# Kernel optimization log

Measured on AMD Instinct MI355X. Metric: run time of the kernel, lower is better.

## Reference

```python
import jax, jax.numpy as jnp
import numpy as np

B, T, S, L = 1, 2048, 512, 1024
C, H, Hk, D = 2048, 16, 4, 128
THETA = 10000.0


def setup_inputs() -> dict:
    key = jax.random.key(0)
    ks = jax.random.split(key, 9)
    sd = 0.02
    return {
        "x": jax.random.normal(ks[0], (B, T, C), jnp.float32),
        "stm": jax.random.normal(ks[1], (B, S, C), jnp.float32),
        "long_q": jax.random.normal(ks[2], (B, L, H, D), jnp.float32),
        "long_k": jax.random.normal(ks[3], (B, L, Hk, D), jnp.float32),
        "long_v": jax.random.normal(ks[4], (B, L, Hk, D), jnp.float32),
        "Wq": jax.random.normal(ks[5], (C, C), jnp.float32) * sd,
        "Wk": jax.random.normal(ks[6], (C, Hk * D), jnp.float32) * sd,
        "Wv": jax.random.normal(ks[7], (C, Hk * D), jnp.float32) * sd,
        "Wo": jax.random.normal(ks[8], (C, C), jnp.float32) * sd,
    }


def _rope_cos_sin(n, d, theta):
    # precompute_freqs_cis: freqs over even dims, angles t*freq
    freqs = 1.0 / (theta ** (jnp.arange(0, d, 2, dtype=jnp.float32) / d))
    ang = jnp.arange(n, dtype=jnp.float32)[:, None] * freqs[None, :]  # (n, d/2)
    return jnp.cos(ang), jnp.sin(ang)


def _apply_rope(x, cos, sin):
    # x: (B, n, h, D); complex-pair rotation over consecutive dims
    x1, x2 = x[..., 0::2], x[..., 1::2]
    c = cos[None, :, None, :]
    s = sin[None, :, None, :]
    r1 = x1 * c - x2 * s
    r2 = x1 * s + x2 * c
    return jnp.stack([r1, r2], axis=-1).reshape(x.shape)


def reference(x, stm, long_q, long_k, long_v, Wq, Wk, Wv, Wo):
    Bb, Tt, Cc = x.shape
    Ss, Ll = stm.shape[1], long_q.shape[1]
    seq = jnp.concatenate([stm, x], axis=1)  # (B, S+T, C)
    q = jnp.concatenate([long_q, (seq @ Wq).reshape(Bb, Ss + Tt, H, D)], axis=1)
    k = jnp.concatenate([long_k, (seq @ Wk).reshape(Bb, Ss + Tt, Hk, D)], axis=1)
    v = jnp.concatenate([long_v, (seq @ Wv).reshape(Bb, Ss + Tt, Hk, D)], axis=1)
    # inline RoPE on the last T+S positions only (memory bank keeps fixed encoding)
    cos, sin = _rope_cos_sin(Ss + Tt, D, THETA)
    q = q.at[:, Ll:].set(_apply_rope(q[:, Ll:], cos, sin))
    k = k.at[:, Ll:].set(_apply_rope(k[:, Ll:], cos, sin))
    tot = Ll + Ss + Tt
    # structured memory mask: causal over full stream, memory keys (< L+S) visible to all
    idx = jnp.arange(tot)
    mask = (idx[None, :] <= idx[:, None]) | (idx[None, :] < Ll + Ss)  # (tot, tot)
    # GQA: repeat_interleave kv heads
    rep = H // Hk
    kr = jnp.repeat(k, rep, axis=2)  # (B, tot, H, D)
    vr = jnp.repeat(v, rep, axis=2)
    att = jnp.einsum("bihd,bjhd->bhij", q, kr) * (1.0 / np.sqrt(D))
    att = jnp.where(mask[None, None], att, -jnp.inf)
    att = jax.nn.softmax(att, axis=-1)
    y = jnp.einsum("bhij,bjhd->bihd", att, vr).reshape(Bb, tot, Cc)
    y = y[:, -Tt:]  # keep only current-block outputs
    return y @ Wo
```

## Files before the change

### kernel.cpp

```cpp
#include <hip/hip_runtime.h>
#include <hip/hip_bf16.h>

typedef __attribute__((ext_vector_type(8))) short short8;
typedef __attribute__((ext_vector_type(4))) short short4v;
typedef __attribute__((ext_vector_type(4))) float f32x4;
typedef __attribute__((ext_vector_type(4))) float float4v;
typedef __attribute__((ext_vector_type(4))) int i32x4;

#define DEVFN static __device__ __forceinline__

#define T_N   2048
#define S_N   512
#define L_N   1024
#define C_N   2048
#define H_N   16
#define HK_N  4
#define D_N   128
#define ST_N  2560
#define TOT_N 3584
#define KV_N  512

DEVFN short f2bf(float f) {
  union { float f; unsigned u; } v; v.f = f;
  return (short)((v.u + 0x7FFFu + ((v.u >> 16) & 1u)) >> 16);
}
DEVFN float bf2f(short s) {
  union { unsigned u; float f; } v; v.u = ((unsigned)(unsigned short)s) << 16;
  return v.f;
}
DEVFN void gload16(const void* g, void* l) {
  __builtin_amdgcn_global_load_lds(
      (__attribute__((address_space(1))) void*)(g),
      (__attribute__((address_space(3))) void*)(l), 16, 0, 0);
}

#define Q_A (S_N * C_N / 4)
#define Q_B (Q_A + T_N * C_N / 4)
#define Q_C (Q_B + L_N * KV_N / 4)
#define Q_D (Q_C + L_N * KV_N / 4)
#define TAB_E (Q_D + ST_N * 64)
__global__ void k_setup(const float* __restrict__ x, const float* __restrict__ stm,
                        const float* __restrict__ lk, const float* __restrict__ lv,
                        short* __restrict__ seq, short* __restrict__ Kf,
                        short* __restrict__ Vf, float* __restrict__ ct,
                        float* __restrict__ st_) {
  int i = blockIdx.x * 256 + threadIdx.x;
  if (i < Q_D) {
    const float* src; short* dst; int off;
    if (i < Q_A)      { src = stm; dst = seq;                         off = i; }
    else if (i < Q_B) { src = x;   dst = seq + (size_t)S_N * C_N;     off = i - Q_A; }
    else if (i < Q_C) { src = lk;  dst = Kf;                          off = i - Q_B; }
    else              { src = lv;  dst = Vf;                          off = i - Q_C; }
    float4v v = reinterpret_cast<const float4v*>(src)[off];
    short4v o;
    o[0] = f2bf(v[0]); o[1] = f2bf(v[1]); o[2] = f2bf(v[2]); o[3] = f2bf(v[3]);
    reinterpret_cast<short4v*>(dst)[off] = o;
  } else {
    int j = i - Q_D;
    int p = j >> 6, fq = j & 63;
    float freq = expf(-(float)fq * (logf(10000.0f) / 64.0f));
    float ang = (float)p * freq;
    ct[j] = cosf(ang);
    st_[j] = sinf(ang);
  }
}

__global__ void k_tconv_all(const float* __restrict__ Wq, const float* __restrict__ Wk,
                            const float* __restrict__ Wv, const float* __restrict__ Wo,
                            short* __restrict__ WqT, short* __restrict__ WkT,
                            short* __restrict__ WvT, short* __restrict__ WoT) {
  __shared__ float tile[32][33];
  const int z = blockIdx.z;
  const float* in = (z == 0) ? Wq : (z == 1) ? Wk : (z == 2) ? Wv : Wo;
  short* outp     = (z == 0) ? WqT : (z == 1) ? WkT : (z == 2) ? WvT : WoT;
  const int cols = (z == 1 || z == 2) ? KV_N : C_N;
  if (blockIdx.x * 32 >= cols) return;
  int c0 = blockIdx.x * 32, r0 = blockIdx.y * 32;
  int tx = threadIdx.x, ty = threadIdx.y;
#pragma unroll
  for (int i = 0; i < 4; i++)
    tile[ty + i * 8][tx] = in[(size_t)(r0 + ty + i * 8) * cols + c0 + tx];
  __syncthreads();
#pragma unroll
  for (int i = 0; i < 4; i++)
    outp[(size_t)(c0 + ty + i * 8) * C_N + r0 + tx] = f2bf(tile[tx][ty + i * 8]);
}

__global__ void k_tv(const short* __restrict__ vf, short* __restrict__ vt) {
  __shared__ short tile[32][33];
  int hk = blockIdx.z;
  int r0 = blockIdx.x * 32;
  int d0 = blockIdx.y * 32;
  int tx = threadIdx.x, ty = threadIdx.y;
#pragma unroll
  for (int i = 0; i < 4; i++)
    tile[ty + i * 8][tx] = vf[(size_t)(r0 + ty + i * 8) * KV_N + hk * D_N + d0 + tx];
  __syncthreads();
  short* o = vt + (size_t)hk * D_N * TOT_N;
#pragma unroll
  for (int i = 0; i < 4; i++)
    o[(size_t)(d0 + ty + i * 8) * TOT_N + r0 + tx] = tile[tx][ty + i * 8];
}

__global__ __launch_bounds__(256) void k_gemm_o(
    const short* __restrict__ A, const short* __restrict__ Bt,
    float* __restrict__ C) {
  __shared__ short lbuf[2 * 6144];
  const int tid = threadIdx.x;
  const int w = tid >> 6, l = tid & 63;
  const int l15 = l & 15, lh = l >> 4;
  const int f0 = blockIdx.x;
  const int f = ((f0 & 7) << 6) + (f0 >> 3);
  const int rb = (f >> 4) << 6, cb = (f & 15) << 7;
  const int wr = (w >> 1) << 5, wc = (w & 1) << 6;
  f32x4 acc[2][4] = {};
  const int cA = tid;
  const short* pa = &A[(size_t)(rb + (cA >> 2)) * 2048 + (((cA ^ (cA >> 2)) & 3) << 3)];
  const int cB0 = tid, cB1 = 256 + tid;
  const short* pb0 = &Bt[(size_t)(cb + (cB0 >> 2)) * 2048 + (((cB0 ^ (cB0 >> 2)) & 3) << 3)];
  const short* pb1 = &Bt[(size_t)(cb + (cB1 >> 2)) * 2048 + (((cB1 ^ (cB1 >> 2)) & 3) << 3)];
  const int offA  = (w * 64) << 4;
  const int offB0 = 4096 + ((w * 64) << 4);
  const int offB1 = 4096 + ((256 + w * 64) << 4);
  char* lbase = (char*)lbuf;
  const int sw = (lh ^ (l15 & 3)) << 3;
  gload16(pa,  lbase + offA);
  gload16(pb0, lbase + offB0);
  gload16(pb1, lbase + offB1);
  int cur = 0;
  for (int kt = 0; kt < 2048; kt += 32) {
    const bool more = (kt + 32 < 2048);
    if (more) {
      char* p = lbase + (cur ^ 1) * 12288;
      gload16(pa  + kt + 32, p + offA);
      gload16(pb0 + kt + 32, p + offB0);
      gload16(pb1 + kt + 32, p + offB1);
      asm volatile("s_waitcnt vmcnt(3)" ::: "memory");
    } else {
      asm volatile("s_waitcnt vmcnt(0)" ::: "memory");
    }
    __builtin_amdgcn_s_barrier();
    __builtin_amdgcn_sched_barrier(0);
    const short* la = (const short*)(lbase + cur * 12288);
    const short* lb = (const short*)(lbase + cur * 12288 + 4096);
    short8 af[2], bg[4];
#pragma unroll
    for (int m = 0; m < 2; m++)
      af[m] = *reinterpret_cast<const short8*>(&la[(wr + m * 16 + l15) * 32 + sw]);
#pragma unroll
    for (int n = 0; n < 4; n++)
      bg[n] = *reinterpret_cast<const short8*>(&lb[(wc + n * 16 + l15) * 32 + sw]);
    __builtin_amdgcn_s_setprio(1);
#pragma unroll
    for (int m = 0; m < 2; m++)
#pragma unroll
      for (int n = 0; n < 4; n++)
        acc[m][n] = __builtin_amdgcn_mfma_f32_16x16x32_bf16(af[m], bg[n], acc[m][n], 0, 0, 0);
    __builtin_amdgcn_s_setprio(0);
    asm volatile("s_waitcnt lgkmcnt(0)" ::: "memory");
    __builtin_amdgcn_sched_barrier(0);
    __builtin_amdgcn_s_barrier();
    __builtin_amdgcn_sched_barrier(0);
    cur ^= 1;
  }
#pragma unroll
  for (int m = 0; m < 2; m++)
#pragma unroll
    for (int n = 0; n < 4; n++)
#pragma unroll
      for (int r = 0; r < 4; r++) {
        int row = rb + wr + m * 16 + lh * 4 + r;
        int col = cb + wc + n * 16 + l15;
        C[(size_t)row * 2048 + col] = acc[m][n][r];
      }
}

__global__ __launch_bounds__(512, 2) void k_gemm_qkv(
    const short* __restrict__ A, const short* __restrict__ Bt,
    short* __restrict__ qbuf, short* __restrict__ Kf, short* __restrict__ Vf,
    const float* __restrict__ ct, const float* __restrict__ st_) {
  __shared__ short lbuf[2 * 12288];
  const int tid = threadIdx.x;
  const int w = tid >> 6, l = tid & 63;
  const int l15 = l & 15, lh = l >> 4;
  const int f0 = blockIdx.x;
  const int f = (f0 % 8) * 26 + f0 / 8;
  int rb, cb;
  if (f < 128) {
    rb = 512 + ((f >> 4) << 8);
    cb = (f & 15) << 7;
  } else {
    int g = f - 128;
    rb = (g >> 3) << 8;
    cb = 2048 + ((g & 7) << 7);
  }
  const int wr = (w >> 1) << 6, wc = (w & 1) << 6;
  f32x4 acc[4][4] = {};
  const int cA0 = tid, cA1 = 512 + tid;
  const short* pa0 = &A[(size_t)(rb + (cA0 >> 2)) * 2048 + (((cA0 ^ (cA0 >> 2)) & 3) << 3)];
  const short* pa1 = &A[(size_t)(rb + (cA1 >> 2)) * 2048 + (((cA1 ^ (cA1 >> 2)) & 3) << 3)];
  const short* pb = &Bt[(size_t)(cb + (tid >> 2)) * 2048 + (((tid ^ (tid >> 2)) & 3) << 3)];
  const int offA0 = (w * 64) << 4;
  const int offA1 = (512 + w * 64) << 4;
  const int offB  = 16384 + ((w * 64) << 4);
  char* lbase = (char*)lbuf;
  const int sw = (lh ^ (l15 & 3)) << 3;
  gload16(pa0, lbase + offA0);
  gload16(pa1, lbase + offA1);
  gload16(pb,  lbase + offB);
  int cur = 0;
  for (int kt = 0; kt < 2048; kt += 32) {
    const bool more = (kt + 32 < 2048);
    if (more) {
      char* p = lbase + (cur ^ 1) * 24576;
      gload16(pa0 + kt + 32, p + offA0);
      gload16(pa1 + kt + 32, p + offA1);
      gload16(pb  + kt + 32, p + offB);
      asm volatile("s_waitcnt vmcnt(3)" ::: "memory");
    } else {
      asm volatile("s_waitcnt vmcnt(0)" ::: "memory");
    }
    __builtin_amdgcn_s_barrier();
    __builtin_amdgcn_sched_barrier(0);
    const short* la = (const short*)(lbase + cur * 24576);
    const short* lb = (const short*)(lbase + cur * 24576 + 16384);
    short8 af[4], bg[4];
#pragma unroll
    for (int m = 0; m < 4; m++)
      af[m] = *reinterpret_cast<const short8*>(&la[(wr + m * 16 + l15) * 32 + sw]);
#pragma unroll
    for (int n = 0; n < 4; n++)
      bg[n] = *reinterpret_cast<const short8*>(&lb[(wc + n * 16 + l15) * 32 + sw]);
    __builtin_amdgcn_s_setprio(1);
#pragma unroll
    for (int m = 0; m < 4; m++)
#pragma unroll
      for (int n = 0; n < 4; n++)
        acc[m][n] = __builtin_amdgcn_mfma_f32_16x16x32_bf16(af[m], bg[n], acc[m][n], 0, 0, 0);
    __builtin_amdgcn_s_setprio(0);
    asm volatile("s_waitcnt lgkmcnt(0)" ::: "memory");
    __builtin_amdgcn_sched_barrier(0);
    __builtin_amdgcn_s_barrier();
    __builtin_amdgcn_sched_barrier(0);
    cur ^= 1;
  }
#pragma unroll
  for (int m = 0; m < 4; m++)
#pragma unroll
    for (int n = 0; n < 4; n++) {
      int coln = cb + wc + n * 16 + l15;
      const bool do_rope = coln < 2560;
      const int fidx = (coln & 127) >> 1;
#pragma unroll
      for (int r = 0; r < 4; r++) {
        int row = rb + wr + m * 16 + lh * 4 + r;
        float v = acc[m][n][r];
        float other = __shfl_xor(v, 1, 64);
        if (do_rope) {
          float co = ct[row * 64 + fidx];
          float si = st_[row * 64 + fidx];
          v = (l15 & 1) ? (other * si + v * co) : (v * co - other * si);
        }
        short bv = f2bf(v);
        if (coln < 2048) {
          qbuf[(size_t)(row - 512) * C_N + coln] = bv;
        } else if (coln < 2560) {
          Kf[(size_t)(L_N + row) * KV_N + (coln - 2048)] = bv;
        } else {
          Vf[(size_t)(L_N + row) * KV_N + (coln - 2560)] = bv;
        }
      }
    }
}

__global__ __launch_bounds__(256, 2) void k_attn(
    const short* __restrict__ Q,
    const short* __restrict__ Kf,
    const short* __restrict__ Vt,
    short* __restrict__ pY,
    float* __restrict__ pM,
    float* __restrict__ pL) {
  __shared__ short kl[64 * 128];
  __shared__ short vl[128 * 64];
  const int f = blockIdx.x;
  const int p = f >> 8;
  const int f8 = f & 255;
  const int hk = f8 & 3;
  const int qraw = (f8 >> 2) & 15;
  const int hh = (f8 >> 6) & 3;
  const int qb = p ? (15 - qraw) : qraw;
  const int h = hk * 4 + hh;
  const int tid = threadIdx.x, w = tid >> 6, l = tid & 63;
  const int l15 = l & 15, lh = l >> 4;
  const int qbase = qb << 7;
  const int qrow0 = qbase + (w << 5);
  short8 aqA[4], aqB[4];
#pragma unroll
  for (int kb = 0; kb < 4; kb++) {
    aqA[kb] = *reinterpret_cast<const short8*>(
        &Q[(size_t)(qrow0 + l15) * C_N + h * D_N + kb * 32 + lh * 8]);
    aqB[kb] = *reinterpret_cast<const short8*>(
        &Q[(size_t)(qrow0 + 16 + l15) * C_N + h * D_N + kb * 32 + lh * 8]);
  }
  short8 ones;
#pragma unroll
  for (int j = 0; j < 8; j++) ones[j] = (short)0x3F80;
  f32x4 yA[8] = {}, yB[8] = {};
  f32x4 lA_ = {}, lB_ = {};
  float mA = -3.0e38f, mB = -3.0e38f;
  const float K2 = 0.12751744f;
  const float THR = 90.0f;
  const int nkt = ((qbase + 1663) >> 6) + 1;
  const int th = nkt >> 1;
  const int t0 = p ? th : 0;
  const int t1 = p ? nkt : th;
  const short* psk[4];
  const short* psv[4];
  int ldsoff[4];
#pragma unroll
  for (int it = 0; it < 4; it++) {
    int c = it * 256 + tid;
    int kr = c >> 4, kkc = c & 15;
    int pkr = (kr & 0x23) | ((kr & 0x0C) << 1) | ((kr >> 2) & 4);
    psk[it] = &Kf[(size_t)pkr * KV_N + hk * D_N + ((kkc ^ (kr & 7)) << 3)];
    int vrow = c >> 3, vkc = c & 7;
    psv[it] = &Vt[(size_t)hk * D_N * TOT_N + (size_t)vrow * TOT_N + ((vkc ^ (vrow & 7)) << 3)];
    ldsoff[it] = (it * 256 + w * 64) << 4;
  }
#pragma unroll
  for (int it = 0; it < 4; it++)
    gload16(psk[it] + (size_t)t0 * 64 * KV_N, (char*)kl + ldsoff[it]);
#pragma unroll
  for (int it = 0; it < 4; it++)
    gload16(psv[it] + (size_t)t0 * 64, (char*)vl + ldsoff[it]);
  __syncthreads();
  for (int t = t0; t < t1; t++) {
    const bool more = (t + 1 < t1);
    short8 kreg[4], vreg[4];
    if (more) {
#pragma unroll
      for (int it = 0; it < 4; it++)
        kreg[it] = *reinterpret_cast<const short8*>(psk[it] + (size_t)(t + 1) * 64 * KV_N);
#pragma unroll
      for (int it = 0; it < 4; it++)
        vreg[it] = *reinterpret_cast<const short8*>(psv[it] + (size_t)(t + 1) * 64);
    }
    f32x4 sA[4] = {}, sB[4] = {};
    __builtin_amdgcn_s_setprio(1);
#pragma unroll
    for (int g = 0; g < 4; g++) {
      int row = g * 16 + l15;
#pragma unroll
      for (int kb = 0; kb < 4; kb++) {
        short8 bk = *reinterpret_cast<const short8*>(
            (const char*)kl + row * 256 + ((((kb << 2) + lh) ^ (row & 7)) << 4));
        sA[g] = __builtin_amdgcn_mfma_f32_16x16x32_bf16(bk, aqA[kb], sA[g], 0, 0, 0);
        sB[g] = __builtin_amdgcn_mfma_f32_16x16x32_bf16(bk, aqB[kb], sB[g], 0, 0, 0);
      }
    }
    __builtin_amdgcn_s_setprio(0);
    if ((t * 64 + 63) > (1536 + qrow0)) {
      int qi = qrow0 + l15;
#pragma unroll
      for (int g = 0; g < 4; g++)
#pragma unroll
        for (int r = 0; r < 4; r++) {
          int key = t * 64 + ((g >> 1) << 5) + (lh << 3) + ((g & 1) << 2) + r;
          if (key > 1536 + qi) sA[g][r] = -3.0e38f;
        }
    }
    if ((t * 64 + 63) > (1536 + qrow0 + 16)) {
      int qi = qrow0 + 16 + l15;
#pragma unroll
      for (int g = 0; g < 4; g++)
#pragma unroll
        for (int r = 0; r < 4; r++) {
          int key = t * 64 + ((g >> 1) << 5) + (lh << 3) + ((g & 1) << 2) + r;
          if (key > 1536 + qi) sB[g][r] = -3.0e38f;
        }
    }
    {
      float lm = sA[0][0];
#pragma unroll
      for (int g = 0; g < 4; g++)
#pragma unroll
        for (int r = 0; r < 4; r++) lm = fmaxf(lm, sA[g][r]);
      if (!__all(lm <= mA + THR)) {
        float rm = fmaxf(lm, __shfl_xor(lm, 16, 64));
        rm = fmaxf(rm, __shfl_xor(rm, 32, 64));
        float mn = fmaxf(mA, rm);
        float scf = __builtin_amdgcn_exp2f((mA - mn) * K2);
        mA = mn;
#pragma unroll
        for (int r = 0; r < 4; r++) {
          float sc_c = __shfl(scf, lh * 4 + r, 64);
          lA_[r] *= sc_c;
#pragma unroll
          for (int dg = 0; dg < 8; dg++) yA[dg][r] *= sc_c;
        }
      }
    }
    {
      float lm = sB[0][0];
#pragma unroll
      for (int g = 0; g < 4; g++)
#pragma unroll
        for (int r = 0; r < 4; r++) lm = fmaxf(lm, sB[g][r]);
      if (!__all(lm <= mB + THR)) {
        float rm = fmaxf(lm, __shfl_xor(lm, 16, 64));
        rm = fmaxf(rm, __shfl_xor(rm, 32, 64));
        float mn = fmaxf(mB, rm);
        float scf = __builtin_amdgcn_exp2f((mB - mn) * K2);
        mB = mn;
#pragma unroll
        for (int r = 0; r < 4; r++) {
          float sc_c = __shfl(scf, lh * 4 + r, 64);
          lB_[r] *= sc_c;
#pragma unroll
          for (int dg = 0; dg < 8; dg++) yB[dg][r] *= sc_c;
        }
      }
    }
    union { i32x4 wv; short8 sv; } uA0, uA1, uB0, uB1;
    {
      const float mk = mA * K2;
      float pvv[16];
#pragma unroll
      for (int g = 0; g < 4; g++)
#pragma unroll
        for (int r = 0; r < 4; r++)
          pvv[g * 4 + r] = __builtin_amdgcn_exp2f(sA[g][r] * K2 - mk);
#pragma unroll
      for (int j = 0; j < 4; j++) {
        unsigned w0, w1;
        int b0 = (j >> 1) * 4 + 2 * (j & 1);
        int b1 = (2 + (j >> 1)) * 4 + 2 * (j & 1);
        asm("v_cvt_pk_bf16_f32 %0, %1, %2" : "=v"(w0) : "v"(pvv[b0]), "v"(pvv[b0 + 1]));
        asm("v_cvt_pk_bf16_f32 %0, %1, %2" : "=v"(w1) : "v"(pvv[b1]), "v"(pvv[b1 + 1]));
        uA0.wv[j] = (int)w0;
        uA1.wv[j] = (int)w1;
      }
    }
    {
      const float mk = mB * K2;
      float pvv[16];
#pragma unroll
      for (int g = 0; g < 4; g++)
#pragma unroll
        for (int r = 0; r < 4; r++)
          pvv[g * 4 + r] = __builtin_amdgcn_exp2f(sB[g][r] * K2 - mk);
#pragma unroll
      for (int j = 0; j < 4; j++) {
        unsigned w0, w1;
        int b0 = (j >> 1) * 4 + 2 * (j & 1);
        int b1 = (2 + (j >> 1)) * 4 + 2 * (j & 1);
        asm("v_cvt_pk_bf16_f32 %0, %1, %2" : "=v"(w0) : "v"(pvv[b0]), "v"(pvv[b0 + 1]));
        asm("v_cvt_pk_bf16_f32 %0, %1, %2" : "=v"(w1) : "v"(pvv[b1]), "v"(pvv[b1 + 1]));
        uB0.wv[j] = (int)w0;
        uB1.wv[j] = (int)w1;
      }
    }
    lA_ = __builtin_amdgcn_mfma_f32_16x16x32_bf16(uA0.sv, ones, lA_, 0, 0, 0);
    lA_ = __builtin_amdgcn_mfma_f32_16x16x32_bf16(uA1.sv, ones, lA_, 0, 0, 0);
    lB_ = __builtin_amdgcn_mfma_f32_16x16x32_bf16(uB0.sv, ones, lB_, 0, 0, 0);
    lB_ = __builtin_amdgcn_mfma_f32_16x16x32_bf16(uB1.sv, ones, lB_, 0, 0, 0);
    __builtin_amdgcn_s_setprio(1);
#pragma unroll
    for (int dg = 0; dg < 8; dg++) {
      int vrow = dg * 16 + l15;
      short8 bv0 = *reinterpret_cast<const short8*>(
          (const char*)vl + (vrow << 7) + ((lh ^ (vrow & 7)) << 4));
      short8 bv1 = *reinterpret_cast<const short8*>(
          (const char*)vl + (vrow << 7) + (((4 + lh) ^ (vrow & 7)) << 4));
      yA[dg] = __builtin_amdgcn_mfma_f32_16x16x32_bf16(uA0.sv, bv0, yA[dg], 0, 0, 0);
      yA[dg] = __builtin_amdgcn_mfma_f32_16x16x32_bf16(uA1.sv, bv1, yA[dg], 0, 0, 0);
      yB[dg] = __builtin_amdgcn_mfma_f32_16x16x32_bf16(uB0.sv, bv0, yB[dg], 0, 0, 0);
      yB[dg] = __builtin_amdgcn_mfma_f32_16x16x32_bf16(uB1.sv, bv1, yB[dg], 0, 0, 0);
    }
    __builtin_amdgcn_s_setprio(0);
    asm volatile("s_waitcnt lgkmcnt(0)" ::: "memory");
    __builtin_amdgcn_sched_barrier(0);
    __builtin_amdgcn_s_barrier();
    __builtin_amdgcn_sched_barrier(0);
    if (more) {
#pragma unroll
      for (int it = 0; it < 4; it++)
        *reinterpret_cast<short8*>((char*)kl + ldsoff[it] + (l << 4)) = kreg[it];
#pragma unroll
      for (int it = 0; it < 4; it++)
        *reinterpret_cast<short8*>((char*)vl + ldsoff[it] + (l << 4)) = vreg[it];
    }
    __syncthreads();
  }
  const size_t base = (size_t)(p * 16 + h) * 2048;
#pragma unroll
  for (int dg = 0; dg < 8; dg++)
#pragma unroll
    for (int r = 0; r < 4; r++) {
      int rowA = qrow0 + lh * 4 + r;
      pY[(base + rowA) * 128 + dg * 16 + l15] = f2bf(yA[dg][r]);
      pY[(base + rowA + 16) * 128 + dg * 16 + l15] = f2bf(yB[dg][r]);
    }
  if (l15 == 0) {
#pragma unroll
    for (int r = 0; r < 4; r++) {
      pL[base + qrow0 + lh * 4 + r] = lA_[r];
      pL[base + qrow0 + 16 + lh * 4 + r] = lB_[r];
    }
  }
  if (lh == 0) {
    pM[base + qrow0 + l15] = mA;
    pM[base + qrow0 + 16 + l15] = mB;
  }
}

__global__ void k_merge(const short* __restrict__ pY, const float* __restrict__ pM,
                        const float* __restrict__ pL, short* __restrict__ Y) {
  const int h = blockIdx.y;
  const int row = blockIdx.x * 16 + (threadIdx.x >> 4);
  const int d0 = (threadIdx.x & 15) * 8;
  const size_t b0 = (size_t)h * 2048 + row;
  const size_t b1 = (size_t)(16 + h) * 2048 + row;
  const float K2 = 0.12751744f;
  float m0 = pM[b0], m1 = pM[b1];
  float l0 = pL[b0], l1 = pL[b1];
  float M = fmaxf(m0, m1);
  float a0 = __builtin_amdgcn_exp2f((m0 - M) * K2);
  float a1 = __builtin_amdgcn_exp2f((m1 - M) * K2);
  float inv = 1.0f / (l0 * a0 + l1 * a1);
  short8 y0 = *reinterpret_cast<const short8*>(&pY[b0 * 128 + d0]);
  short8 y1 = *reinterpret_cast<const short8*>(&pY[b1 * 128 + d0]);
  short8 o;
#pragma unroll
  for (int j = 0; j < 8; j++)
    o[j] = f2bf((bf2f(y0[j]) * a0 + bf2f(y1[j]) * a1) * inv);
  *reinterpret_cast<short8*>(&Y[(size_t)row * C_N + h * D_N + d0]) = o;
}

extern "C" void kernel_launch(void* const* d_in, const int* in_sizes, int n_in,
                              void* d_out, int out_size, void* d_ws, size_t ws_size,
                              hipStream_t stream) {
  const float* x      = (const float*)d_in[0];
  const float* stm    = (const float*)d_in[1];
  const float* long_k = (const float*)d_in[3];
  const float* long_v = (const float*)d_in[4];
  const float* Wq     = (const float*)d_in[5];
  const float* Wk     = (const float*)d_in[6];
  const float* Wv     = (const float*)d_in[7];
  const float* Wo     = (const float*)d_in[8];
  float* out = (float*)d_out;

  short* seq  = (short*)d_ws;
  short* WqT  = seq  + (size_t)ST_N * C_N;
  short* WkT  = WqT  + (size_t)C_N * C_N;
  short* WvT  = WkT  + (size_t)KV_N * C_N;
  short* WoT  = WvT  + (size_t)KV_N * C_N;
  short* qbuf = WoT  + (size_t)C_N * C_N;
  short* Kf   = qbuf + (size_t)T_N * C_N;
  short* Vf   = Kf   + (size_t)TOT_N * KV_N;
  short* Vt   = Vf   + (size_t)TOT_N * KV_N;
  short* ybuf = Vt   + (size_t)TOT_N * KV_N;
  float* ctab = (float*)(ybuf + (size_t)T_N * C_N);
  float* stab = ctab + (size_t)ST_N * 64;

  short* pY = (short*)d_ws;
  float* pM = (float*)(pY + (size_t)2 * 16 * 2048 * 128);
  float* pL = pM + (size_t)2 * 16 * 2048;

  k_setup<<<TAB_E / 256, 256, 0, stream>>>(x, stm, long_k, long_v, seq, Kf, Vf, ctab, stab);

  k_tconv_all<<<dim3(64, 64, 4), dim3(32, 8), 0, stream>>>(
      Wq, Wk, Wv, Wo, WqT, WkT, WvT, WoT);

  k_gemm_qkv<<<208, 512, 0, stream>>>(seq, WqT, qbuf, Kf, Vf, ctab, stab);

  k_tv<<<dim3(TOT_N / 32, D_N / 32, HK_N), dim3(32, 8), 0, stream>>>(Vf, Vt);

  k_attn<<<512, 256, 0, stream>>>(qbuf, Kf, Vt, pY, pM, pL);

  k_merge<<<dim3(128, 16), 256, 0, stream>>>(pY, pM, pL, ybuf);

  k_gemm_o<<<512, 256, 0, stream>>>(ybuf, WoT, out);
}
```

Measured before the change: 169.7 us.

## Switch GEMM mainloops to register-staged prefetch and double-buffer attention K/V LDS

Both GEMM kernels stop using asynchronous direct global-to-LDS loads for the next K tile. They now prefetch the tile into registers before the MFMA work, write it into the alternate LDS buffer afterwards, and use a single __syncthreads per iteration. The attention kernel gets two LDS buffers for K and V, so the next tile is written to the spare buffer and the second barrier per tile goes away. The aim is fewer barriers and better overlap of loads with compute. The cost is more registers and LDS, plus losing the direct-to-LDS path in the GEMMs.

```diff
diff --git a/kernel.cpp b/kernel.cpp
--- a/kernel.cpp
+++ b/kernel.cpp
@@ -127,20 +127,16 @@
   gload16(pa,  lbase + offA);
   gload16(pb0, lbase + offB0);
   gload16(pb1, lbase + offB1);
-  int cur = 0;
-  for (int kt = 0; kt < 2048; kt += 32) {
+  for (int kt = 0, i = 0; kt < 2048; kt += 32, i++) {
+    const int cur = i & 1;
+    __syncthreads();
     const bool more = (kt + 32 < 2048);
+    short8 ra, rb0, rb1;
     if (more) {
-      char* p = lbase + (cur ^ 1) * 12288;
-      gload16(pa  + kt + 32, p + offA);
-      gload16(pb0 + kt + 32, p + offB0);
-      gload16(pb1 + kt + 32, p + offB1);
-      asm volatile("s_waitcnt vmcnt(3)" ::: "memory");
-    } else {
-      asm volatile("s_waitcnt vmcnt(0)" ::: "memory");
-    }
-    __builtin_amdgcn_s_barrier();
-    __builtin_amdgcn_sched_barrier(0);
+      ra  = *reinterpret_cast<const short8*>(pa  + kt + 32);
+      rb0 = *reinterpret_cast<const short8*>(pb0 + kt + 32);
+      rb1 = *reinterpret_cast<const short8*>(pb1 + kt + 32);
+    }
     const short* la = (const short*)(lbase + cur * 12288);
     const short* lb = (const short*)(lbase + cur * 12288 + 4096);
     short8 af[2], bg[4];
@@ -157,11 +153,12 @@
       for (int n = 0; n < 4; n++)
         acc[m][n] = __builtin_amdgcn_mfma_f32_16x16x32_bf16(af[m], bg[n], acc[m][n], 0, 0, 0);
     __builtin_amdgcn_s_setprio(0);
-    asm volatile("s_waitcnt lgkmcnt(0)" ::: "memory");
-    __builtin_amdgcn_sched_barrier(0);
-    __builtin_amdgcn_s_barrier();
-    __builtin_amdgcn_sched_barrier(0);
-    cur ^= 1;
+    if (more) {
+      char* p = lbase + (cur ^ 1) * 12288;
+      *reinterpret_cast<short8*>(p + offA  + (l << 4)) = ra;
+      *reinterpret_cast<short8*>(p + offB0 + (l << 4)) = rb0;
+      *reinterpret_cast<short8*>(p + offB1 + (l << 4)) = rb1;
+    }
   }
 #pragma unroll
   for (int m = 0; m < 2; m++)
@@ -208,20 +205,16 @@
   gload16(pa0, lbase + offA0);
   gload16(pa1, lbase + offA1);
   gload16(pb,  lbase + offB);
-  int cur = 0;
-  for (int kt = 0; kt < 2048; kt += 32) {
+  for (int kt = 0, i = 0; kt < 2048; kt += 32, i++) {
+    const int cur = i & 1;
+    __syncthreads();
     const bool more = (kt + 32 < 2048);
+    short8 ra0, ra1, rbv;
     if (more) {
-      char* p = lbase + (cur ^ 1) * 24576;
-      gload16(pa0 + kt + 32, p + offA0);
-      gload16(pa1 + kt + 32, p + offA1);
-      gload16(pb  + kt + 32, p + offB);
-      asm volatile("s_waitcnt vmcnt(3)" ::: "memory");
-    } else {
-      asm volatile("s_waitcnt vmcnt(0)" ::: "memory");
-    }
-    __builtin_amdgcn_s_barrier();
-    __builtin_amdgcn_sched_barrier(0);
+      ra0 = *reinterpret_cast<const short8*>(pa0 + kt + 32);
+      ra1 = *reinterpret_cast<const short8*>(pa1 + kt + 32);
+      rbv = *reinterpret_cast<const short8*>(pb  + kt + 32);
+    }
     const short* la = (const short*)(lbase + cur * 24576);
     const short* lb = (const short*)(lbase + cur * 24576 + 16384);
     short8 af[4], bg[4];
@@ -238,11 +231,12 @@
       for (int n = 0; n < 4; n++)
         acc[m][n] = __builtin_amdgcn_mfma_f32_16x16x32_bf16(af[m], bg[n], acc[m][n], 0, 0, 0);
     __builtin_amdgcn_s_setprio(0);
-    asm volatile("s_waitcnt lgkmcnt(0)" ::: "memory");
-    __builtin_amdgcn_sched_barrier(0);
-    __builtin_amdgcn_s_barrier();
-    __builtin_amdgcn_sched_barrier(0);
-    cur ^= 1;
+    if (more) {
+      char* p = lbase + (cur ^ 1) * 24576;
+      *reinterpret_cast<short8*>(p + offA0 + (l << 4)) = ra0;
+      *reinterpret_cast<short8*>(p + offA1 + (l << 4)) = ra1;
+      *reinterpret_cast<short8*>(p + offB  + (l << 4)) = rbv;
+    }
   }
 #pragma unroll
   for (int m = 0; m < 4; m++)
@@ -280,8 +274,8 @@
     short* __restrict__ pY,
     float* __restrict__ pM,
     float* __restrict__ pL) {
-  __shared__ short kl[64 * 128];
-  __shared__ short vl[128 * 64];
+  __shared__ short kl[2][64 * 128];
+  __shared__ short vl[2][128 * 64];
   const int f = blockIdx.x;
   const int p = f >> 8;
   const int f8 = f & 255;
@@ -333,8 +327,9 @@
 #pragma unroll
   for (int it = 0; it < 4; it++)
     gload16(psv[it] + (size_t)t0 * 64, (char*)vl + ldsoff[it]);
-  __syncthreads();
   for (int t = t0; t < t1; t++) {
+    const int cur = (t - t0) & 1;
+    __syncthreads();
     const bool more = (t + 1 < t1);
     short8 kreg[4], vreg[4];
     if (more) {
@@ -345,6 +340,8 @@
       for (int it = 0; it < 4; it++)
         vreg[it] = *reinterpret_cast<const short8*>(psv[it] + (size_t)(t + 1) * 64);
     }
+    const char* kbuf = (const char*)kl + cur * 16384;
+    const char* vbuf = (const char*)vl + cur * 16384;
     f32x4 sA[4] = {}, sB[4] = {};
     __builtin_amdgcn_s_setprio(1);
 #pragma unroll
@@ -353,7 +350,7 @@
 #pragma unroll
       for (int kb = 0; kb < 4; kb++) {
         short8 bk = *reinterpret_cast<const short8*>(
-            (const char*)kl + row * 256 + ((((kb << 2) + lh) ^ (row & 7)) << 4));
+            kbuf + row * 256 + ((((kb << 2) + lh) ^ (row & 7)) << 4));
         sA[g] = __builtin_amdgcn_mfma_f32_16x16x32_bf16(bk, aqA[kb], sA[g], 0, 0, 0);
         sB[g] = __builtin_amdgcn_mfma_f32_16x16x32_bf16(bk, aqB[kb], sB[g], 0, 0, 0);
       }
@@ -469,28 +466,25 @@
     for (int dg = 0; dg < 8; dg++) {
       int vrow = dg * 16 + l15;
       short8 bv0 = *reinterpret_cast<const short8*>(
-          (const char*)vl + (vrow << 7) + ((lh ^ (vrow & 7)) << 4));
+          vbuf + (vrow << 7) + ((lh ^ (vrow & 7)) << 4));
       short8 bv1 = *reinterpret_cast<const short8*>(
-          (const char*)vl + (vrow << 7) + (((4 + lh) ^ (vrow & 7)) << 4));
+          vbuf + (vrow << 7) + (((4 + lh) ^ (vrow & 7)) << 4));
       yA[dg] = __builtin_amdgcn_mfma_f32_16x16x32_bf16(uA0.sv, bv0, yA[dg], 0, 0, 0);
       yA[dg] = __builtin_amdgcn_mfma_f32_16x16x32_bf16(uA1.sv, bv1, yA[dg], 0, 0, 0);
       yB[dg] = __builtin_amdgcn_mfma_f32_16x16x32_bf16(uB0.sv, bv0, yB[dg], 0, 0, 0);
       yB[dg] = __builtin_amdgcn_mfma_f32_16x16x32_bf16(uB1.sv, bv1, yB[dg], 0, 0, 0);
     }
     __builtin_amdgcn_s_setprio(0);
-    asm volatile("s_waitcnt lgkmcnt(0)" ::: "memory");
-    __builtin_amdgcn_sched_barrier(0);
-    __builtin_amdgcn_s_barrier();
-    __builtin_amdgcn_sched_barrier(0);
     if (more) {
+      char* kw = (char*)kl + (cur ^ 1) * 16384;
+      char* vw = (char*)vl + (cur ^ 1) * 16384;
 #pragma unroll
       for (int it = 0; it < 4; it++)
-        *reinterpret_cast<short8*>((char*)kl + ldsoff[it] + (l << 4)) = kreg[it];
+        *reinterpret_cast<short8*>(kw + ldsoff[it] + (l << 4)) = kreg[it];
 #pragma unroll
       for (int it = 0; it < 4; it++)
-        *reinterpret_cast<short8*>((char*)vl + ldsoff[it] + (l << 4)) = vreg[it];
-    }
-    __syncthreads();
+        *reinterpret_cast<short8*>(vw + ldsoff[it] + (l << 4)) = vreg[it];
+    }
   }
   const size_t base = (size_t)(p * 16 + h) * 2048;
 #pragma unroll
```

New measurement: 174.2 us. 1.03x slower.
